# Performance work log

Measured on AMD Instinct MI355X. Metric: run time of the kernel, lower is better.

## Reference

```python
import jax, jax.numpy as jnp
import numpy as np

B, S, E, H = 2, 2048, 1024, 16
HD = E // H


def setup_inputs() -> dict:
    key = jax.random.key(0)
    ks = jax.random.split(key, 5)
    scale = 1.0 / np.sqrt(E)
    return {
        "query": jax.random.normal(ks[0], (B, S, E), jnp.float32),
        "key": jax.random.normal(ks[1], (B, S, E), jnp.float32),
        "value": jax.random.normal(ks[2], (B, S, E), jnp.float32),
        "qkv_w": jax.random.normal(ks[3], (3 * E, E), jnp.float32) * scale,
        "qkv_b": jnp.zeros((3 * E,), jnp.float32),
        "out_w": jax.random.normal(ks[4], (E, E), jnp.float32) * scale,
        "out_b": jnp.zeros((E,), jnp.float32),
    }


def reference(query, key, value, qkv_w, qkv_b, out_w, out_b):
    # Fused QKV projection from query (module ignores key/value contents)
    qkv = query @ qkv_w.T + qkv_b                      # [B,S,3E]
    qkv = qkv.reshape(B, S, 3, H, HD)
    q = qkv[:, :, 0].transpose(0, 2, 1, 3)             # [B,H,S,HD]
    k = qkv[:, :, 1].transpose(0, 2, 1, 3)
    v = qkv[:, :, 2].transpose(0, 2, 1, 3)
    scaling = 1.0 / np.sqrt(HD)
    scores = jnp.einsum("bhqd,bhkd->bhqk", q, k) * scaling  # [B,H,S,S]
    probs = jax.nn.softmax(scores, axis=-1)
    ctx = jnp.einsum("bhqk,bhkd->bhqd", probs, v)      # [B,H,S,HD]
    ctx = ctx.transpose(0, 2, 1, 3).reshape(B, S, E)
    return ctx @ out_w.T + out_b
```

## Files before the change

kernel.cpp:

```cpp
#include <hip/hip_runtime.h>
#include <hip/hip_bf16.h>
#include <math.h>

#define BB 2
#define SS 2048
#define EE 1024
#define HH 16
#define HD 64

typedef __bf16 bf16;
typedef __bf16 bf16x8 __attribute__((ext_vector_type(8)));
typedef float floatx4 __attribute__((ext_vector_type(4)));

#define MFMA(a, b, c) __builtin_amdgcn_mfma_f32_16x16x32_bf16(a, b, c, 0, 0, 0)

__device__ inline void async16(const bf16* g, bf16* l) {
    __builtin_amdgcn_global_load_lds(
        (const __attribute__((address_space(1))) void*)g,
        (__attribute__((address_space(3))) void*)l, 16, 0, 0);
}

__global__ __launch_bounds__(256) void cvt3(
    const float* __restrict__ a, const float* __restrict__ b,
    const float* __restrict__ c,
    bf16* __restrict__ oa, bf16* __restrict__ ob, bf16* __restrict__ oc) {
    const long NA = (long)4096 * 1024, NB = (long)3072 * 1024, NC = (long)1024 * 1024;
    const long total = (NA + NB + NC) >> 2;
    long i = (long)blockIdx.x * blockDim.x + threadIdx.x;
    const long stride = (long)gridDim.x * blockDim.x;
    for (; i < total; i += stride) {
        const long e = i << 2;
        const float* src;
        bf16* dst;
        if (e < NA)           { src = a + e;            dst = oa + e; }
        else if (e < NA + NB) { src = b + (e - NA);     dst = ob + (e - NA); }
        else                  { src = c + (e - NA - NB); dst = oc + (e - NA - NB); }
        float4 v = *(const float4*)src;
        union { bf16 h[4]; uint2 u; } t;
        t.h[0] = (bf16)v.x; t.h[1] = (bf16)v.y; t.h[2] = (bf16)v.z; t.h[3] = (bf16)v.w;
        *(uint2*)dst = t.u;
    }
}

__global__ __launch_bounds__(256) void qkv_gemm(
    const bf16* __restrict__ A, const bf16* __restrict__ W,
    const float* __restrict__ bias,
    bf16* __restrict__ Qw, bf16* __restrict__ Kw, bf16* __restrict__ Vtw) {
    __shared__ __align__(16) bf16 As[128 * 64];
    __shared__ __align__(16) bf16 Bs[128 * 64];
    const int tid  = threadIdx.x;
    const int wave = tid >> 6, lane = tid & 63;
    const int quad = lane >> 4, l16 = lane & 15;
    const int wr = wave >> 1, wc = wave & 1;
    const int m0 = blockIdx.y * 128, n0 = blockIdx.x * 128;
    const int lr = lane >> 3;
    const int lc = (lane & 7) * 8;

    const bf16* Ag = A + (long)(m0 + wave * 32 + lr) * 1024 + lc;
    const bf16* Bg = W + (long)(n0 + wave * 32 + lr) * 1024 + lc;
    bf16* Al = As + (wave * 32) * 64 + lane * 8;
    bf16* Bl = Bs + (wave * 32) * 64 + lane * 8;

    floatx4 acc[4][4] = {};

    for (int k0 = 0; k0 < 1024; k0 += 64) {
        __syncthreads();
#pragma unroll
        for (int j = 0; j < 4; ++j) {
            async16(Ag + (long)j * 8 * 1024 + k0, Al + j * 8 * 64);
            async16(Bg + (long)j * 8 * 1024 + k0, Bl + j * 8 * 64);
        }
        __syncthreads();
#pragma unroll
        for (int c = 0; c < 2; ++c) {
            bf16x8 af[4], bfr[4];
#pragma unroll
            for (int mi = 0; mi < 4; ++mi)
                af[mi] = *(const bf16x8*)&As[(wr * 64 + mi * 16 + l16) * 64 + c * 32 + quad * 8];
#pragma unroll
            for (int ni = 0; ni < 4; ++ni)
                bfr[ni] = *(const bf16x8*)&Bs[(wc * 64 + ni * 16 + l16) * 64 + c * 32 + quad * 8];
#pragma unroll
            for (int mi = 0; mi < 4; ++mi)
#pragma unroll
                for (int ni = 0; ni < 4; ++ni)
                    acc[mi][ni] = MFMA(af[mi], bfr[ni], acc[mi][ni]);
        }
    }

#pragma unroll
    for (int mi = 0; mi < 4; ++mi)
#pragma unroll
        for (int ni = 0; ni < 4; ++ni) {
            const int n = n0 + wc * 64 + ni * 16 + l16;
            const float bn = bias[n];
            const int sel = n >> 10;
            const int e = n & 1023, h = e >> 6, d = e & 63;
            if (sel == 2) {
                const int m_base = m0 + wr * 64 + mi * 16 + quad * 4;
                const int b = m_base >> 11, s0 = m_base & 2047;
                union { bf16 h4[4]; uint2 u; } t;
#pragma unroll
                for (int r = 0; r < 4; ++r)
                    t.h4[r] = (bf16)(acc[mi][ni][r] + bn);
                *(uint2*)&Vtw[((long)(b * HH + h) * HD + d) * SS + s0] = t.u;
            } else {
#pragma unroll
                for (int r = 0; r < 4; ++r) {
                    const int m = m0 + wr * 64 + mi * 16 + quad * 4 + r;
                    const int b = m >> 11, s = m & 2047;
                    const float v = acc[mi][ni][r] + bn;
                    if (sel == 0)
                        Qw[((long)(b * HH + h) * SS + s) * HD + d] = (bf16)(v * 0.125f);
                    else
                        Kw[((long)(b * HH + h) * SS + s) * HD + d] = (bf16)v;
                }
            }
        }
}

__global__ __launch_bounds__(256) void attn(
    const bf16* __restrict__ Qw, const bf16* __restrict__ Kw,
    const bf16* __restrict__ Vtw, bf16* __restrict__ ctxw) {
    __shared__ __align__(16) bf16 Kt[64][72];
    __shared__ __align__(16) bf16 Vt[64][72];
    __shared__ __align__(16) bf16 Pl[4][32][72];

    const int tid  = threadIdx.x;
    const int wave = tid >> 6, lane = tid & 63;
    const int quad = lane >> 4, l16 = lane & 15;
    const int qb = blockIdx.x, bh = blockIdx.y;
    const bf16* Qh = Qw  + (long)bh * SS * HD;
    const bf16* Kh = Kw  + (long)bh * SS * HD;
    const bf16* Vh = Vtw + (long)bh * HD * SS;

    const int qbase = qb * 128 + wave * 32;
    bf16x8 qf[2][2];
#pragma unroll
    for (int g = 0; g < 2; ++g)
#pragma unroll
        for (int c = 0; c < 2; ++c)
            qf[g][c] = *(const bf16x8*)&Qh[(long)(qbase + g * 16 + l16) * HD + c * 32 + quad * 8];

    floatx4 ctx[2][4] = {};
    float lrun[2][4] = {{0.f,0.f,0.f,0.f},{0.f,0.f,0.f,0.f}};

    const int srow = tid >> 2;
    const int sc0  = (tid & 3) * 16;

    uint4 kr0, kr1, vr0, vr1;
    {
        const uint4* ks = (const uint4*)&Kh[(long)srow * HD + sc0];
        kr0 = ks[0]; kr1 = ks[1];
        const uint4* vs = (const uint4*)&Vh[(long)srow * SS + sc0];
        vr0 = vs[0]; vr1 = vs[1];
    }

    for (int kt = 0; kt < 32; ++kt) {
        __syncthreads();
        *(uint4*)&Kt[srow][sc0]     = kr0;
        *(uint4*)&Kt[srow][sc0 + 8] = kr1;
        *(uint4*)&Vt[srow][sc0]     = vr0;
        *(uint4*)&Vt[srow][sc0 + 8] = vr1;
        __syncthreads();

        if (kt < 31) {
            const uint4* ks = (const uint4*)&Kh[(long)((kt + 1) * 64 + srow) * HD + sc0];
            kr0 = ks[0]; kr1 = ks[1];
            const uint4* vs = (const uint4*)&Vh[(long)srow * SS + (kt + 1) * 64 + sc0];
            vr0 = vs[0]; vr1 = vs[1];
        }

        floatx4 sf[2][4];
#pragma unroll
        for (int j = 0; j < 4; ++j) {
            bf16x8 kf0 = *(const bf16x8*)&Kt[j * 16 + l16][quad * 8];
            bf16x8 kf1 = *(const bf16x8*)&Kt[j * 16 + l16][32 + quad * 8];
#pragma unroll
            for (int g = 0; g < 2; ++g) {
                floatx4 t = {0.f, 0.f, 0.f, 0.f};
                t = MFMA(qf[g][0], kf0, t);
                sf[g][j] = MFMA(qf[g][1], kf1, t);
            }
        }

#pragma unroll
        for (int g = 0; g < 2; ++g)
#pragma unroll
            for (int j = 0; j < 4; ++j)
#pragma unroll
                for (int r = 0; r < 4; ++r) {
                    const float p = __expf(sf[g][j][r]);
                    sf[g][j][r] = p;
                    lrun[g][r] += p;
                }

#pragma unroll
        for (int g = 0; g < 2; ++g)
#pragma unroll
            for (int j = 0; j < 4; ++j)
#pragma unroll
                for (int r = 0; r < 4; ++r)
                    Pl[wave][g * 16 + quad * 4 + r][j * 16 + l16] = (bf16)sf[g][j][r];

#pragma unroll
        for (int kc = 0; kc < 2; ++kc) {
            bf16x8 vf[4];
#pragma unroll
            for (int dt = 0; dt < 4; ++dt)
                vf[dt] = *(const bf16x8*)&Vt[dt * 16 + l16][kc * 32 + quad * 8];
#pragma unroll
            for (int g = 0; g < 2; ++g) {
                bf16x8 pf = *(const bf16x8*)&Pl[wave][g * 16 + l16][kc * 32 + quad * 8];
#pragma unroll
                for (int dt = 0; dt < 4; ++dt)
                    ctx[g][dt] = MFMA(pf, vf[dt], ctx[g][dt]);
            }
        }
    }

    const int b = bh >> 4, h = bh & 15;
#pragma unroll
    for (int g = 0; g < 2; ++g)
#pragma unroll
        for (int r = 0; r < 4; ++r) {
            float rs = lrun[g][r];
#pragma unroll
            for (int off = 1; off < 16; off <<= 1) rs += __shfl_xor(rs, off, 64);
            const float inv = 1.0f / rs;
            const int qg = qbase + g * 16 + quad * 4 + r;
#pragma unroll
            for (int dt = 0; dt < 4; ++dt) {
                const int d = dt * 16 + l16;
                ctxw[((long)b * SS + qg) * EE + h * HD + d] = (bf16)(ctx[g][dt][r] * inv);
            }
        }
}

__global__ __launch_bounds__(256) void out_gemm(
    const bf16* __restrict__ A, const bf16* __restrict__ W,
    const float* __restrict__ bias, float* __restrict__ out) {
    __shared__ __align__(16) bf16 As[64 * 64];
    __shared__ __align__(16) bf16 Bs[128 * 64];
    const int tid  = threadIdx.x;
    const int wave = tid >> 6, lane = tid & 63;
    const int quad = lane >> 4, l16 = lane & 15;
    const int wr = wave & 1, wc = wave >> 1;
    const int m0 = blockIdx.y * 64, n0 = blockIdx.x * 128;
    const int lr = lane >> 3;
    const int lc = (lane & 7) * 8;

    const bf16* Ag = A + (long)(m0 + wave * 16 + lr) * 1024 + lc;
    const bf16* Bg = W + (long)(n0 + wave * 32 + lr) * 1024 + lc;
    bf16* Al = As + (wave * 16) * 64 + lane * 8;
    bf16* Bl = Bs + (wave * 32) * 64 + lane * 8;

    floatx4 acc[2][4] = {};

    for (int k0 = 0; k0 < 1024; k0 += 64) {
        __syncthreads();
#pragma unroll
        for (int j = 0; j < 2; ++j)
            async16(Ag + (long)j * 8 * 1024 + k0, Al + j * 8 * 64);
#pragma unroll
        for (int j = 0; j < 4; ++j)
            async16(Bg + (long)j * 8 * 1024 + k0, Bl + j * 8 * 64);
        __syncthreads();
#pragma unroll
        for (int c = 0; c < 2; ++c) {
            bf16x8 af[2], bfr[4];
#pragma unroll
            for (int mi = 0; mi < 2; ++mi)
                af[mi] = *(const bf16x8*)&As[(wr * 32 + mi * 16 + l16) * 64 + c * 32 + quad * 8];
#pragma unroll
            for (int ni = 0; ni < 4; ++ni)
                bfr[ni] = *(const bf16x8*)&Bs[(wc * 64 + ni * 16 + l16) * 64 + c * 32 + quad * 8];
#pragma unroll
            for (int mi = 0; mi < 2; ++mi)
#pragma unroll
                for (int ni = 0; ni < 4; ++ni)
                    acc[mi][ni] = MFMA(af[mi], bfr[ni], acc[mi][ni]);
        }
    }

#pragma unroll
    for (int mi = 0; mi < 2; ++mi)
#pragma unroll
        for (int ni = 0; ni < 4; ++ni) {
            const int n = n0 + wc * 64 + ni * 16 + l16;
            const float bn = bias[n];
#pragma unroll
            for (int r = 0; r < 4; ++r) {
                const int m = m0 + wr * 32 + mi * 16 + quad * 4 + r;
                out[(long)m * 1024 + n] = acc[mi][ni][r] + bn;
            }
        }
}

extern "C" void kernel_launch(void* const* d_in, const int* in_sizes, int n_in,
                              void* d_out, int out_size, void* d_ws, size_t ws_size,
                              hipStream_t stream) {
    const float* query = (const float*)d_in[0];
    const float* qkv_w = (const float*)d_in[3];
    const float* qkv_b = (const float*)d_in[4];
    const float* out_w = (const float*)d_in[5];
    const float* out_b = (const float*)d_in[6];

    const long NTOK = (long)BB * SS;
    bf16* qb   = (bf16*)d_ws;
    bf16* wqb  = qb  + NTOK * EE;
    bf16* owb  = wqb + (long)3 * EE * EE;
    bf16* Qw   = owb + (long)EE * EE;
    bf16* Kw   = Qw  + NTOK * EE;
    bf16* Vtw  = Kw  + NTOK * EE;
    bf16* ctxw = qb;
    float* out = (float*)d_out;

    cvt3<<<2048, 256, 0, stream>>>(query, qkv_w, out_w, qb, wqb, owb);
    qkv_gemm<<<dim3(24, 32), 256, 0, stream>>>(qb, wqb, qkv_b, Qw, Kw, Vtw);
    attn<<<dim3(16, 32), 256, 0, stream>>>(Qw, Kw, Vtw, ctxw);
    out_gemm<<<dim3(8, 64), 256, 0, stream>>>(ctxw, owb, out_b, out);
}
```

Baseline: 234.7 us.

## Restructure attention to 32x32 MFMA with transposed scores and register-resident P

Rewrites the attention kernel to compute S^T = K·Q^T with 32x32x16 MFMAs so each lane holds one query column. The probabilities are packed to bf16 and rearranged across lane halves with permlane32 swaps, so they feed the P·V MFMA directly instead of round-tripping through a shared-memory P buffer. K/V tiles move to an XOR-swizzled unpadded LDS layout, and the row-sum reduction shrinks to a single shuffle. This removes the per-tile LDS writes and reads for P and the padding, at the cost of inline asm that depends on gfx950-specific instructions and a more complex output indexing.

```diff
diff --git a/kernel.cpp b/kernel.cpp
--- a/kernel.cpp
+++ b/kernel.cpp
@@ -11,13 +11,21 @@
 typedef __bf16 bf16;
 typedef __bf16 bf16x8 __attribute__((ext_vector_type(8)));
 typedef float floatx4 __attribute__((ext_vector_type(4)));
+typedef float floatx16 __attribute__((ext_vector_type(16)));
 
 #define MFMA(a, b, c) __builtin_amdgcn_mfma_f32_16x16x32_bf16(a, b, c, 0, 0, 0)
+#define MFMA32(a, b, c) __builtin_amdgcn_mfma_f32_32x32x16_bf16(a, b, c, 0, 0, 0)
 
 __device__ inline void async16(const bf16* g, bf16* l) {
     __builtin_amdgcn_global_load_lds(
         (const __attribute__((address_space(1))) void*)g,
         (__attribute__((address_space(3))) void*)l, 16, 0, 0);
+}
+
+__device__ inline unsigned cvt_pk_bf16(float a, float b) {
+    unsigned r;
+    asm("v_cvt_pk_bf16_f32 %0, %1, %2" : "=v"(r) : "v"(a), "v"(b));
+    return r;
 }
 
 __global__ __launch_bounds__(256) void cvt3(
@@ -122,31 +130,34 @@
 __global__ __launch_bounds__(256) void attn(
     const bf16* __restrict__ Qw, const bf16* __restrict__ Kw,
     const bf16* __restrict__ Vtw, bf16* __restrict__ ctxw) {
-    __shared__ __align__(16) bf16 Kt[64][72];
-    __shared__ __align__(16) bf16 Vt[64][72];
-    __shared__ __align__(16) bf16 Pl[4][32][72];
-
-    const int tid  = threadIdx.x;
+    __shared__ __align__(16) bf16 Kt[64 * 64];
+    __shared__ __align__(16) bf16 Vt[64 * 64];
+
+    const int tid = threadIdx.x;
     const int wave = tid >> 6, lane = tid & 63;
-    const int quad = lane >> 4, l16 = lane & 15;
+    const int l5 = lane & 31, hi = lane >> 5;
     const int qb = blockIdx.x, bh = blockIdx.y;
     const bf16* Qh = Qw  + (long)bh * SS * HD;
     const bf16* Kh = Kw  + (long)bh * SS * HD;
     const bf16* Vh = Vtw + (long)bh * HD * SS;
 
     const int qbase = qb * 128 + wave * 32;
-    bf16x8 qf[2][2];
-#pragma unroll
-    for (int g = 0; g < 2; ++g)
-#pragma unroll
-        for (int c = 0; c < 2; ++c)
-            qf[g][c] = *(const bf16x8*)&Qh[(long)(qbase + g * 16 + l16) * HD + c * 32 + quad * 8];
-
-    floatx4 ctx[2][4] = {};
-    float lrun[2][4] = {{0.f,0.f,0.f,0.f},{0.f,0.f,0.f,0.f}};
+    bf16x8 qf[4];
+#pragma unroll
+    for (int d0 = 0; d0 < 4; ++d0)
+        qf[d0] = *(const bf16x8*)&Qh[(long)(qbase + l5) * HD + d0 * 16 + hi * 8];
+
+    floatx16 ctx0 = {}, ctx1 = {};
+    float lsum = 0.f;
 
     const int srow = tid >> 2;
     const int sc0  = (tid & 3) * 16;
+    const int swz  = (srow & 7) << 3;
+    const int rswz = (l5 & 7) << 3;
+    bf16* Kl0 = &Kt[srow * 64 + (sc0 ^ swz)];
+    bf16* Kl1 = &Kt[srow * 64 + ((sc0 + 8) ^ swz)];
+    bf16* Vl0 = &Vt[srow * 64 + (sc0 ^ swz)];
+    bf16* Vl1 = &Vt[srow * 64 + ((sc0 + 8) ^ swz)];
 
     uint4 kr0, kr1, vr0, vr1;
     {
@@ -158,10 +169,10 @@
 
     for (int kt = 0; kt < 32; ++kt) {
         __syncthreads();
-        *(uint4*)&Kt[srow][sc0]     = kr0;
-        *(uint4*)&Kt[srow][sc0 + 8] = kr1;
-        *(uint4*)&Vt[srow][sc0]     = vr0;
-        *(uint4*)&Vt[srow][sc0 + 8] = vr1;
+        *(uint4*)Kl0 = kr0;
+        *(uint4*)Kl1 = kr1;
+        *(uint4*)Vl0 = vr0;
+        *(uint4*)Vl1 = vr1;
         __syncthreads();
 
         if (kt < 31) {
@@ -171,70 +182,61 @@
             vr0 = vs[0]; vr1 = vs[1];
         }
 
-        floatx4 sf[2][4];
-#pragma unroll
-        for (int j = 0; j < 4; ++j) {
-            bf16x8 kf0 = *(const bf16x8*)&Kt[j * 16 + l16][quad * 8];
-            bf16x8 kf1 = *(const bf16x8*)&Kt[j * 16 + l16][32 + quad * 8];
-#pragma unroll
-            for (int g = 0; g < 2; ++g) {
-                floatx4 t = {0.f, 0.f, 0.f, 0.f};
-                t = MFMA(qf[g][0], kf0, t);
-                sf[g][j] = MFMA(qf[g][1], kf1, t);
-            }
-        }
-
-#pragma unroll
-        for (int g = 0; g < 2; ++g)
-#pragma unroll
-            for (int j = 0; j < 4; ++j)
-#pragma unroll
-                for (int r = 0; r < 4; ++r) {
-                    const float p = __expf(sf[g][j][r]);
-                    sf[g][j][r] = p;
-                    lrun[g][r] += p;
-                }
-
-#pragma unroll
-        for (int g = 0; g < 2; ++g)
-#pragma unroll
-            for (int j = 0; j < 4; ++j)
-#pragma unroll
-                for (int r = 0; r < 4; ++r)
-                    Pl[wave][g * 16 + quad * 4 + r][j * 16 + l16] = (bf16)sf[g][j][r];
-
-#pragma unroll
-        for (int kc = 0; kc < 2; ++kc) {
-            bf16x8 vf[4];
-#pragma unroll
-            for (int dt = 0; dt < 4; ++dt)
-                vf[dt] = *(const bf16x8*)&Vt[dt * 16 + l16][kc * 32 + quad * 8];
-#pragma unroll
-            for (int g = 0; g < 2; ++g) {
-                bf16x8 pf = *(const bf16x8*)&Pl[wave][g * 16 + l16][kc * 32 + quad * 8];
-#pragma unroll
-                for (int dt = 0; dt < 4; ++dt)
-                    ctx[g][dt] = MFMA(pf, vf[dt], ctx[g][dt]);
-            }
-        }
-    }
+        floatx16 sf[2];
+#pragma unroll
+        for (int kb = 0; kb < 2; ++kb) {
+            floatx16 s = {};
+#pragma unroll
+            for (int d0 = 0; d0 < 4; ++d0) {
+                const bf16x8 af = *(const bf16x8*)
+                    &Kt[(kb * 32 + l5) * 64 + ((d0 * 16 + hi * 8) ^ rswz)];
+                s = MFMA32(af, qf[d0], s);
+            }
+            sf[kb] = s;
+        }
+
+#pragma unroll
+        for (int kb = 0; kb < 2; ++kb) {
+#pragma unroll
+            for (int r = 0; r < 16; ++r) {
+                const float p = __expf(sf[kb][r]);
+                sf[kb][r] = p;
+                lsum += p;
+            }
+            unsigned w[8];
+#pragma unroll
+            for (int i = 0; i < 8; ++i)
+                w[i] = cvt_pk_bf16(sf[kb][2 * i], sf[kb][2 * i + 1]);
+            asm("v_permlane32_swap_b32 %0, %1" : "+v"(w[0]), "+v"(w[2]));
+            asm("v_permlane32_swap_b32 %0, %1" : "+v"(w[1]), "+v"(w[3]));
+            asm("v_permlane32_swap_b32 %0, %1" : "+v"(w[4]), "+v"(w[6]));
+            asm("v_permlane32_swap_b32 %0, %1" : "+v"(w[5]), "+v"(w[7]));
+            union { unsigned u[4]; bf16x8 v; } pa0 = {{w[0], w[1], w[2], w[3]}},
+                                               pa1 = {{w[4], w[5], w[6], w[7]}};
+#pragma unroll
+            for (int kc = 0; kc < 2; ++kc) {
+                const bf16x8 pa = kc ? pa1.v : pa0.v;
+                const int kcol = kb * 32 + kc * 16 + hi * 8;
+                const bf16x8 vf0 = *(const bf16x8*)&Vt[l5 * 64 + (kcol ^ rswz)];
+                const bf16x8 vf1 = *(const bf16x8*)&Vt[(32 + l5) * 64 + (kcol ^ rswz)];
+                ctx0 = MFMA32(pa, vf0, ctx0);
+                ctx1 = MFMA32(pa, vf1, ctx1);
+            }
+        }
+    }
+
+    const float rs  = lsum + __shfl_xor(lsum, 32, 64);
+    const float inv = 1.0f / rs;
 
     const int b = bh >> 4, h = bh & 15;
 #pragma unroll
-    for (int g = 0; g < 2; ++g)
-#pragma unroll
-        for (int r = 0; r < 4; ++r) {
-            float rs = lrun[g][r];
-#pragma unroll
-            for (int off = 1; off < 16; off <<= 1) rs += __shfl_xor(rs, off, 64);
-            const float inv = 1.0f / rs;
-            const int qg = qbase + g * 16 + quad * 4 + r;
-#pragma unroll
-            for (int dt = 0; dt < 4; ++dt) {
-                const int d = dt * 16 + l16;
-                ctxw[((long)b * SS + qg) * EE + h * HD + d] = (bf16)(ctx[g][dt][r] * inv);
-            }
-        }
+    for (int r = 0; r < 16; ++r) {
+        const int qrow = (r & 3) + 8 * (r >> 2) + 4 * hi;
+        const float iq = __shfl(inv, qrow, 64);
+        const long base = ((long)b * SS + qbase + qrow) * EE + h * HD;
+        ctxw[base + l5]      = (bf16)(ctx0[r] * iq);
+        ctxw[base + 32 + l5] = (bf16)(ctx1[r] * iq);
+    }
 }
 
 __global__ __launch_bounds__(256) void out_gemm(
```

Result: faster. 224.2 us (-4.5%).
